# Performance work log

Measured on AMD Instinct MI355X. Metric: run time of the kernel, lower is better.

## Reference

```python
import jax, jax.numpy as jnp
import numpy as np

POOL = 7
H, W, C = 200, 200, 512
NUM_ROIS = 128


def setup_inputs() -> dict:
    key = jax.random.key(0)
    k1, k2, k3 = jax.random.split(key, 3)
    img = jax.random.normal(k1, (1, H, W, C), dtype=jnp.float32)
    # (x, y, w, h) in feature-map pixels; w,h >= POOL+1 so every bin is >=1px,
    # and x+w <= W, y+h <= H so crops stay in bounds (as the original assumes).
    wh = jax.random.uniform(k2, (1, NUM_ROIS, 2), minval=float(POOL + 1), maxval=64.0)
    xy = jax.random.uniform(k3, (1, NUM_ROIS, 2)) * (jnp.array([W, H], jnp.float32) - wh)
    rois = jnp.concatenate([xy, wh], axis=-1).astype(jnp.float32)
    return {"img": img, "rois": rois, "pool_size": POOL}


def _roi_pool(x, rois, P):
    # x: (H, W, C) feature map; rois: (R, 4) as (x, y, w, h) floats.
    h_dim, w_dim, _ = x.shape
    ks = jnp.arange(P + 1, dtype=jnp.float32)
    rows = jnp.arange(h_dim)
    cols = jnp.arange(w_dim)

    def pool_one(roi):
        rx, ry, rw, rh = roi[0], roi[1], roi[2], roi[3]
        # Bin boundaries: original computes x1 = int(x + ix*w/P), x2 = int(x + (ix+1)*w/P),
        # i.e. contiguous non-overlapping segments [b[k], b[k+1]).
        bx = (rx + ks * (rw / P)).astype(jnp.int32)
        by = (ry + ks * (rh / P)).astype(jnp.int32)
        # Map each row/col to its bin id; out-of-roi pixels -> dummy segment P.
        rid = jnp.searchsorted(by, rows, side='right') - 1
        rid = jnp.where((rid < 0) | (rid >= P), P, rid)
        cid = jnp.searchsorted(bx, cols, side='right') - 1
        cid = jnp.where((cid < 0) | (cid >= P), P, cid)
        # Max-reduce rows into y-bins, then cols into x-bins (separable rect max).
        rm = jax.ops.segment_max(x, rid, num_segments=P + 1)                     # (P+1, W, C) [jy, w, c]
        cm = jax.ops.segment_max(rm.transpose(1, 0, 2), cid, num_segments=P + 1)  # (P+1, P+1, C) [ix, jy, c]
        return cm[:P, :P].transpose(1, 0, 2)  # (jy, ix, c)

    return jax.vmap(pool_one)(rois)  # (R, P, P, C)


def reference(img, rois, pool_size):
    # Output: (1, num_rois, pool_size, pool_size, channels), tf dim ordering.
    out = _roi_pool(img[0], rois[0], pool_size)
    return out[None]
```

## Files before the change

kernel.cpp:

```cpp
#include <hip/hip_runtime.h>


#define IMG_H 200
#define IMG_W 200
#define IMG_C 512
#define C4 (IMG_C / 4)
#define POOL 7
#define NROI 128
#define PLANES 4
#define NXCD 8
#define NBIN (POOL * POOL)
#define NITEM (NROI * NBIN)
#define SLOTS_PER_XCD (NITEM / NXCD)

typedef float f4v __attribute__((ext_vector_type(4)));

__device__ __forceinline__ float4 max4(float4 a, float4 b) {
    return make_float4(fmaxf(a.x, b.x), fmaxf(a.y, b.y),
                       fmaxf(a.z, b.z), fmaxf(a.w, b.w));
}

__device__ __forceinline__ int imin(int a, int b) { return a < b ? a : b; }
__device__ __forceinline__ int imax(int a, int b) { return a > b ? a : b; }

__device__ __forceinline__ unsigned spread8(unsigned x) {
    x &= 0xFFu;
    x = (x | (x << 4)) & 0x0F0Fu;
    x = (x | (x << 2)) & 0x3333u;
    x = (x | (x << 1)) & 0x5555u;
    return x;
}

__global__ __launch_bounds__(PLANES * 128, 8) void roi_pool_kernel(
    const float* __restrict__ img,
    const float* __restrict__ rois,
    float* __restrict__ out)
{
    __shared__ unsigned short s_key[NROI];
    __shared__ float          s_areaROI[NROI];
    __shared__ int            s_rank[NROI];
    __shared__ unsigned char  s_perm[NROI];
    __shared__ float          s_area[NROI];
    __shared__ float          s_pref[NROI];
    __shared__ int            s_chunk[NROI];
    __shared__ int            s_rstart[NXCD];
    __shared__ int            s_len[NXCD];
    __shared__ int            s_spillpre[NXCD + 1];
    __shared__ int            s_freepre[NXCD + 1];
    __shared__ int            s_roi, s_bin;
    __shared__ float4         red[PLANES - 1][C4];

    const int tid = threadIdx.x;
    const int t   = tid & 127;
    const int seg = tid >> 7;

    if (seg == 0) {
        const float rx = rois[t * 4 + 0];
        const float ry = rois[t * 4 + 1];
        const float rw = rois[t * 4 + 2];
        const float rh = rois[t * 4 + 3];
        const unsigned cx = (unsigned)(int)(rx + 0.5f * rw);
        const unsigned cy = (unsigned)(int)(ry + 0.5f * rh);
        s_key[t] = (unsigned short)((spread8(cy) << 1) | spread8(cx));
        s_areaROI[t] = rw * rh;
        s_rank[t] = 0;
    }
    if (tid < NXCD) s_len[tid] = 0;
    __syncthreads();

    {
        const unsigned my = s_key[t];
        int r = 0;
        const int u0 = seg * 32;
        #pragma unroll 8
        for (int u = u0; u < u0 + 32; ++u) {
            const unsigned ku = s_key[u];
            r += (int)((ku < my) | ((ku == my) & (u < t)));
        }
        atomicAdd(&s_rank[t], r);
    }
    __syncthreads();

    if (seg == 0) {
        const int r = s_rank[t];
        s_perm[r] = (unsigned char)t;
        s_area[r] = s_areaROI[t];
    }
    __syncthreads();

    if (seg == 0) {
        float v = s_area[t];
        #pragma unroll
        for (int d = 1; d < 64; d <<= 1) {
            const float o = __shfl_up(v, d);
            if ((t & 63) >= d) v += o;
        }
        s_pref[t] = v;
    }
    __syncthreads();

    if (seg == 0) {
        const float w0tot = s_pref[63];
        const float pre   = s_pref[t] + ((t >= 64) ? w0tot : 0.f);
        const float total = s_pref[127] + w0tot;
        const float mid = pre - 0.5f * s_area[t];
        const int c = imin((int)(mid * ((float)NXCD / total)), NXCD - 1);
        s_chunk[t] = c;
        atomicAdd(&s_len[c], NBIN);
    }
    __syncthreads();

    if (seg == 0) {
        const int c = s_chunk[t];
        if (t == 0 || s_chunk[t - 1] != c) s_rstart[c] = t;
    }
    if (tid == 0) {
        int sp = 0, fp = 0;
        #pragma unroll
        for (int x = 0; x < NXCD; ++x) {
            s_spillpre[x] = sp;
            s_freepre[x]  = fp;
            sp += imax(0, s_len[x] - SLOTS_PER_XCD);
            fp += imax(0, SLOTS_PER_XCD - s_len[x]);
        }
        s_spillpre[NXCD] = sp;
        s_freepre[NXCD]  = fp;
    }
    __syncthreads();

    if (tid == 0) {
        const int x = blockIdx.x & (NXCD - 1);
        const int j = blockIdx.x >> 3;
        int tt, mm;
        if (j < s_len[x]) {
            tt = s_rstart[x] + j / NBIN;
            mm = j % NBIN;
        } else {
            const int si = s_freepre[x] + (j - s_len[x]);
            int xx = 0;
            while (!(si >= s_spillpre[xx] && si < s_spillpre[xx + 1])) ++xx;
            const int jj = SLOTS_PER_XCD + (si - s_spillpre[xx]);
            tt = s_rstart[xx] + jj / NBIN;
            mm = jj % NBIN;
        }
        s_roi = (int)s_perm[tt];
        s_bin = mm;
    }
    __syncthreads();

    const int roi = s_roi;
    const int bin = s_bin;
    const int jy = bin / POOL;
    const int ix = bin % POOL;

    const float rx = rois[roi * 4 + 0];
    const float ry = rois[roi * 4 + 1];
    const float rw = rois[roi * 4 + 2];
    const float rh = rois[roi * 4 + 3];

    const float sx = __fdiv_rn(rw, 7.0f);
    const float sy = __fdiv_rn(rh, 7.0f);
    const int x1 = (int)__fadd_rn(rx, __fmul_rn((float)ix,       sx));
    const int x2 = (int)__fadd_rn(rx, __fmul_rn((float)(ix + 1), sx));
    const int y1 = (int)__fadd_rn(ry, __fmul_rn((float)jy,       sy));
    const int y2 = (int)__fadd_rn(ry, __fmul_rn((float)(jy + 1), sy));

    const int c4 = tid & 127;
    const int p  = tid >> 7;
    const float4* __restrict__ img4 = (const float4*)img;

    const int bw = x2 - x1;
    const int area = bw * (y2 - y1);

    const float4 NEG = make_float4(-INFINITY, -INFINITY, -INFINITY, -INFINITY);
    float4 m = NEG;

    int dx = p, dy = 0;
    while (dx >= bw) { dx -= bw; ++dy; }
    #pragma unroll 2
    for (int i = p; i < area; i += PLANES) {
        const size_t px = (size_t)(y1 + dy) * IMG_W + (size_t)(x1 + dx);
        m = max4(m, img4[px * C4 + c4]);
        dx += PLANES;
        while (dx >= bw) { dx -= bw; ++dy; }
    }

    if (p > 0) red[p - 1][c4] = m;
    __syncthreads();
    if (p == 0) {
        m = max4(m, red[0][c4]);
        m = max4(m, red[1][c4]);
        m = max4(m, red[2][c4]);

        float4* __restrict__ out4 = (float4*)out;
        f4v* __restrict__ dst =
            (f4v*)&out4[((size_t)(roi * POOL + jy) * POOL + ix) * C4 + c4];
        __builtin_nontemporal_store(*(const f4v*)&m, dst);
    }
}

extern "C" void kernel_launch(void* const* d_in, const int* in_sizes, int n_in,
                              void* d_out, int out_size, void* d_ws, size_t ws_size,
                              hipStream_t stream) {
    (void)in_sizes; (void)n_in; (void)d_ws; (void)ws_size; (void)out_size;
    const float* img  = (const float*)d_in[0];
    const float* rois = (const float*)d_in[1];
    float* out = (float*)d_out;

    roi_pool_kernel<<<dim3(NITEM), dim3(PLANES * 128), 0, stream>>>(
        img, rois, out);
}
```

Before: 145.1 us.

## Process a whole row of pool bins per block instead of one bin

Each block now handles one ROI's full bin row (7 bins) rather than a single bin, so there are 7x fewer blocks. The four planes split image rows instead of flat pixels, and each thread keeps 7 accumulators that are reduced through a larger shared buffer. The aim is to amortise the per-block ROI sort and schedule setup and to drop the per-pixel div/mod stepping. In exchange there are fewer blocks (896), more registers and LDS per block, and load imbalance when a bin has fewer than four rows.

```diff
diff --git a/kernel.cpp b/kernel.cpp
--- a/kernel.cpp
+++ b/kernel.cpp
@@ -7,11 +7,10 @@
 #define C4 (IMG_C / 4)
 #define POOL 7
 #define NROI 128
-#define PLANES 4
 #define NXCD 8
-#define NBIN (POOL * POOL)
-#define NITEM (NROI * NBIN)
-#define SLOTS_PER_XCD (NITEM / NXCD)
+#define JPB  POOL
+#define NBLK (NROI * JPB)
+#define SLOTS_PER_XCD (NBLK / NXCD)
 
 typedef float f4v __attribute__((ext_vector_type(4)));
 
@@ -31,7 +30,7 @@
     return x;
 }
 
-__global__ __launch_bounds__(PLANES * 128, 8) void roi_pool_kernel(
+__global__ __launch_bounds__(512, 4) void roi_pool_kernel(
     const float* __restrict__ img,
     const float* __restrict__ rois,
     float* __restrict__ out)
@@ -47,8 +46,8 @@
     __shared__ int            s_len[NXCD];
     __shared__ int            s_spillpre[NXCD + 1];
     __shared__ int            s_freepre[NXCD + 1];
-    __shared__ int            s_roi, s_bin;
-    __shared__ float4         red[PLANES - 1][C4];
+    __shared__ int            s_roi, s_jy;
+    __shared__ float4         red[3][POOL][C4];
 
     const int tid = threadIdx.x;
     const int t   = tid & 127;
@@ -106,7 +105,7 @@
         const float mid = pre - 0.5f * s_area[t];
         const int c = imin((int)(mid * ((float)NXCD / total)), NXCD - 1);
         s_chunk[t] = c;
-        atomicAdd(&s_len[c], NBIN);
+        atomicAdd(&s_len[c], JPB);
     }
     __syncthreads();
 
@@ -132,26 +131,25 @@
         const int x = blockIdx.x & (NXCD - 1);
         const int j = blockIdx.x >> 3;
         int tt, mm;
-        if (j < s_len[x]) {
-            tt = s_rstart[x] + j / NBIN;
-            mm = j % NBIN;
+        const int lenx = s_len[x];
+        if (j < lenx) {
+            tt = s_rstart[x] + j / JPB;
+            mm = j % JPB;
         } else {
-            const int si = s_freepre[x] + (j - s_len[x]);
+            const int si = s_freepre[x] + (j - lenx);
             int xx = 0;
             while (!(si >= s_spillpre[xx] && si < s_spillpre[xx + 1])) ++xx;
             const int jj = SLOTS_PER_XCD + (si - s_spillpre[xx]);
-            tt = s_rstart[xx] + jj / NBIN;
-            mm = jj % NBIN;
+            tt = s_rstart[xx] + jj / JPB;
+            mm = jj % JPB;
         }
         s_roi = (int)s_perm[tt];
-        s_bin = mm;
+        s_jy  = mm;
     }
     __syncthreads();
 
     const int roi = s_roi;
-    const int bin = s_bin;
-    const int jy = bin / POOL;
-    const int ix = bin % POOL;
+    const int jy  = s_jy;
 
     const float rx = rois[roi * 4 + 0];
     const float ry = rois[roi * 4 + 1];
@@ -160,8 +158,6 @@
 
     const float sx = __fdiv_rn(rw, 7.0f);
     const float sy = __fdiv_rn(rh, 7.0f);
-    const int x1 = (int)__fadd_rn(rx, __fmul_rn((float)ix,       sx));
-    const int x2 = (int)__fadd_rn(rx, __fmul_rn((float)(ix + 1), sx));
     const int y1 = (int)__fadd_rn(ry, __fmul_rn((float)jy,       sy));
     const int y2 = (int)__fadd_rn(ry, __fmul_rn((float)(jy + 1), sy));
 
@@ -169,33 +165,38 @@
     const int p  = tid >> 7;
     const float4* __restrict__ img4 = (const float4*)img;
 
-    const int bw = x2 - x1;
-    const int area = bw * (y2 - y1);
-
     const float4 NEG = make_float4(-INFINITY, -INFINITY, -INFINITY, -INFINITY);
-    float4 m = NEG;
-
-    int dx = p, dy = 0;
-    while (dx >= bw) { dx -= bw; ++dy; }
-    #pragma unroll 2
-    for (int i = p; i < area; i += PLANES) {
-        const size_t px = (size_t)(y1 + dy) * IMG_W + (size_t)(x1 + dx);
-        m = max4(m, img4[px * C4 + c4]);
-        dx += PLANES;
-        while (dx >= bw) { dx -= bw; ++dy; }
-    }
-
-    if (p > 0) red[p - 1][c4] = m;
+    float4 m[POOL];
+
+    #pragma unroll
+    for (int ix = 0; ix < POOL; ++ix) {
+        const int x1 = (int)__fadd_rn(rx, __fmul_rn((float)ix,       sx));
+        const int x2 = (int)__fadd_rn(rx, __fmul_rn((float)(ix + 1), sx));
+        float4 acc = NEG;
+        for (int yy = y1 + p; yy < y2; yy += 4) {
+            const float4* __restrict__ row = img4 + ((size_t)yy * IMG_W) * C4 + c4;
+            #pragma unroll 4
+            for (int x = x1; x < x2; ++x)
+                acc = max4(acc, row[(size_t)x * C4]);
+        }
+        m[ix] = acc;
+    }
+
+    if (p > 0) {
+        #pragma unroll
+        for (int ix = 0; ix < POOL; ++ix) red[p - 1][ix][c4] = m[ix];
+    }
     __syncthreads();
     if (p == 0) {
-        m = max4(m, red[0][c4]);
-        m = max4(m, red[1][c4]);
-        m = max4(m, red[2][c4]);
-
         float4* __restrict__ out4 = (float4*)out;
-        f4v* __restrict__ dst =
-            (f4v*)&out4[((size_t)(roi * POOL + jy) * POOL + ix) * C4 + c4];
-        __builtin_nontemporal_store(*(const f4v*)&m, dst);
+        #pragma unroll
+        for (int ix = 0; ix < POOL; ++ix) {
+            float4 mm = max4(max4(m[ix], red[0][ix][c4]),
+                             max4(red[1][ix][c4], red[2][ix][c4]));
+            f4v* __restrict__ dst =
+                (f4v*)&out4[((size_t)(roi * POOL + jy) * POOL + ix) * C4 + c4];
+            __builtin_nontemporal_store(*(const f4v*)&mm, dst);
+        }
     }
 }
 
@@ -207,6 +208,5 @@
     const float* rois = (const float*)d_in[1];
     float* out = (float*)d_out;
 
-    roi_pool_kernel<<<dim3(NITEM), dim3(PLANES * 128), 0, stream>>>(
-        img, rois, out);
-}
+    roi_pool_kernel<<<dim3(NBLK), dim3(512), 0, stream>>>(img, rois, out);
+}
```

Result: slower. 156.2 us (+7.6%).
